# Optimization experiments

Measured on AMD Instinct MI355X. Metric: run time of the kernel, lower is better.

## Reference

```python
import jax, jax.numpy as jnp
import numpy as np

T = 524288
INPUT_LEN = 64
N_MEMORY = 64
OUTPUT_LEN = 32


def setup_inputs() -> dict:
    key = jax.random.key(0)
    k_x, k_w1, k_b1, k_w2, k_b2 = jax.random.split(key, 5)
    s = 0.05  # tf.random_normal_initializer default stddev
    return {
        "inputs": jax.random.normal(k_x, (T, INPUT_LEN), dtype=jnp.float32),
        "W1": s * jax.random.normal(k_w1, (INPUT_LEN, 2 * N_MEMORY), dtype=jnp.float32),
        "B1": s * jax.random.normal(k_b1, (1, 2 * N_MEMORY), dtype=jnp.float32),
        "W2": s * jax.random.normal(k_w2, (N_MEMORY, OUTPUT_LEN), dtype=jnp.float32),
        "B2": s * jax.random.normal(k_b2, (1, OUTPUT_LEN), dtype=jnp.float32),
    }


def reference(inputs, W1, B1, W2, B2):
    n_memory = W2.shape[0]
    # gates: h = sigmoid(x W1 + B1), split into left/right halves  [T, M] each
    h = jax.nn.sigmoid(inputs @ W1 + B1)
    left, right = jnp.split(h, 2, axis=1)
    prod = left * right
    # affine linear recurrence: u_t = prod_{t-1} * u_{t-1} + (1 - left_{t-1}), u_0 = 0
    a = prod[:-1]            # [T-1, M] multiplicative coeffs
    b = 1.0 - left[:-1]      # [T-1, M] additive terms

    def step(u, ab):
        a_t, b_t = ab
        u = a_t * u + b_t
        return u, u

    u0 = jnp.zeros((n_memory,), dtype=inputs.dtype)
    _, us = jax.lax.scan(step, u0, (a, b))
    z = jnp.concatenate([u0[None, :], us], axis=0)  # [T, M]
    out = z @ W2 + B2                               # [T, output_len]
    return out
```

## Files before the change

### kernel.cpp

```cpp
#include <hip/hip_runtime.h>

#define TT    524288
#define CHUNK 512
#define NCH   (TT / CHUNK)
#define SUB   64
#define NSUB  (CHUNK / SUB)

typedef __attribute__((ext_vector_type(8))) short short8;
typedef __attribute__((ext_vector_type(4))) float f32x4;

__device__ __forceinline__ unsigned short f2bf(float f) {
    union { float f; unsigned u; } v; v.f = f;
    unsigned r = v.u + 0x7FFFu + ((v.u >> 16) & 1u);
    return (unsigned short)(r >> 16);
}
__device__ __forceinline__ unsigned packbf2(float a, float b) {
    union { float f; unsigned u; } va, vb; va.f = a; vb.f = b;
    unsigned ra = va.u + 0x7FFFu + ((va.u >> 16) & 1u);
    unsigned rb = vb.u + 0x7FFFu + ((vb.u >> 16) & 1u);
    return (ra >> 16) | (rb & 0xFFFF0000u);
}
__device__ __forceinline__ float2 unpackbf2(unsigned w) {
    union { unsigned u; float f; } a, b;
    a.u = w << 16; b.u = w & 0xFFFF0000u;
    return make_float2(a.f, b.f);
}
__device__ __forceinline__ float sigf(float v) {
    return __builtin_amdgcn_rcpf(1.0f + __expf(-v));
}

union U8 { uint4 u4; short8 s8; };

__global__ __launch_bounds__(256, 3)
void aphase(const float* __restrict__ x, const float* __restrict__ W1,
            const float* __restrict__ B1,
            float* __restrict__ Aout, float* __restrict__ Bout,
            uint4* __restrict__ abg)
{
    __shared__ __align__(16) short W1t[128 * 72];
    __shared__ float    B1s[128];
    __shared__ float    segA[32 * 66], segB[32 * 66];

    const int tid  = threadIdx.x;
    const int c    = blockIdx.x;
    const int wave = tid >> 6;
    const int lane = tid & 63;
    const int quad = lane >> 4;
    const int lr   = lane & 15;

    for (int i = tid; i < 2048; i += 256) {
        float4 w4 = ((const float4*)W1)[i];
        int k = i >> 5, n0 = (i & 31) * 4;
        W1t[(n0 + 0) * 72 + k] = (short)f2bf(w4.x);
        W1t[(n0 + 1) * 72 + k] = (short)f2bf(w4.y);
        W1t[(n0 + 2) * 72 + k] = (short)f2bf(w4.z);
        W1t[(n0 + 3) * 72 + k] = (short)f2bf(w4.w);
    }
    if (tid < 128) B1s[tid] = B1[tid];
    __syncthreads();

    float bb[8];
    #pragma unroll
    for (int j = 0; j < 8; ++j) bb[j] = B1s[j * 16 + lr];

    const float* xbase = x + (size_t)c * CHUNK * 64;

    #define FRAGP(ss, rt) ((const float4*)(xbase + (size_t)(((ss) * 64 + (rt) * 16 + lr)) * 64) + quad * 2)

    const float4* p0 = FRAGP(wave, 0);
    float4 c0 = p0[0], c1 = p0[1], c2 = p0[8], c3 = p0[9];

    const bool h1 = (quad & 1) != 0;
    const bool h2 = (quad & 2) != 0;

    for (int fi = 0; fi < 8; ++fi) {
        const int ss = (fi < 4) ? wave : (wave + 4);
        const int rt = fi & 3;

        U8 ua, ub;
        ua.u4 = make_uint4(packbf2(c0.x, c0.y), packbf2(c0.z, c0.w),
                           packbf2(c1.x, c1.y), packbf2(c1.z, c1.w));
        ub.u4 = make_uint4(packbf2(c2.x, c2.y), packbf2(c2.z, c2.w),
                           packbf2(c3.x, c3.y), packbf2(c3.z, c3.w));
        const short8 a0 = ua.s8, a1 = ub.s8;

        if (fi < 7) {
            const int ns = (fi + 1 < 4) ? wave : (wave + 4);
            const int nr = (fi + 1) & 3;
            const float4* np = FRAGP(ns, nr);
            c0 = np[0]; c1 = np[1]; c2 = np[8]; c3 = np[9];
        }

        f32x4 acc[8];
        #pragma unroll
        for (int j = 0; j < 8; ++j) {
            acc[j][0] = bb[j]; acc[j][1] = bb[j]; acc[j][2] = bb[j]; acc[j][3] = bb[j];
        }
        #pragma unroll
        for (int j = 0; j < 8; ++j) {
            const short8 b0 = *(const short8*)&W1t[(j * 16 + lr) * 72 + quad * 8];
            const short8 b1 = *(const short8*)&W1t[(j * 16 + lr) * 72 + quad * 8 + 32];
            acc[j] = __builtin_amdgcn_mfma_f32_16x16x32_bf16(a0, b0, acc[j], 0, 0, 0);
            acc[j] = __builtin_amdgcn_mfma_f32_16x16x32_bf16(a1, b1, acc[j], 0, 0, 0);
        }

        unsigned pk[4][4];
        #pragma unroll
        for (int j = 0; j < 4; ++j) {
            #pragma unroll
            for (int r = 0; r < 4; ++r) {
                float hl = sigf(acc[j][r]);
                float hr = sigf(acc[j + 4][r]);
                pk[j][r] = packbf2(hl * hr, 1.0f - hl);
            }
        }

        {
            uint4* dstq = abg + ((size_t)((c * NSUB + ss) * 16 + rt * 4 + quad)) * 64 + lr;
            #pragma unroll
            for (int j = 0; j < 4; ++j)
                dstq[j * 16] = make_uint4(pk[j][0], pk[j][1], pk[j][2], pk[j][3]);
        }

        float Aa[4], Ba[4];
        #pragma unroll
        for (int j = 0; j < 4; ++j) {
            float A = 1.0f, Bv = 0.0f;
            #pragma unroll
            for (int r = 0; r < 4; ++r) {
                float2 f = unpackbf2(pk[j][r]);
                Bv = fmaf(f.x, Bv, f.y); A *= f.x;
            }
            Aa[j] = A; Ba[j] = Bv;
        }
        #pragma unroll
        for (int j = 0; j < 4; ++j) {
            float Ap = __shfl_xor(Aa[j], 16);
            float Bp = __shfl_xor(Ba[j], 16);
            float Ahi = h1 ? Aa[j] : Ap;
            float Blo = h1 ? Bp    : Ba[j];
            float Bhi = h1 ? Ba[j] : Bp;
            Aa[j] *= Ap;
            Ba[j] = fmaf(Ahi, Blo, Bhi);

            Ap = __shfl_xor(Aa[j], 32);
            Bp = __shfl_xor(Ba[j], 32);
            Ahi = h2 ? Aa[j] : Ap;
            Blo = h2 ? Bp    : Ba[j];
            Bhi = h2 ? Ba[j] : Bp;
            Aa[j] *= Ap;
            Ba[j] = fmaf(Ahi, Blo, Bhi);
        }
        const float Asel = (quad == 0) ? Aa[0] : (quad == 1) ? Aa[1]
                         : (quad == 2) ? Aa[2] : Aa[3];
        const float Bsel = (quad == 0) ? Ba[0] : (quad == 1) ? Ba[1]
                         : (quad == 2) ? Ba[2] : Ba[3];
        const int band = ss * 4 + rt;
        segA[band * 66 + lane] = Asel;
        segB[band * 66 + lane] = Bsel;
    }
    #undef FRAGP

    __syncthreads();
    if (tid < 64) {
        float sA = 1.0f, sB = 0.0f;
        for (int b = 0; b < 32; ++b) {
            float A2 = segA[b * 66 + tid], B2v = segB[b * 66 + tid];
            sB = fmaf(A2, sB, B2v); sA *= A2;
        }
        Aout[c * 64 + tid] = sA; Bout[c * 64 + tid] = sB;
    }
}

__global__ void carry_scan(const float* __restrict__ Aar, const float* __restrict__ Bar,
                           float* __restrict__ carry)
{
    __shared__ float sA[16 * 66], sB[16 * 66];
    const int tid = threadIdx.x;
    const int ch = tid & 63, seg = tid >> 6;
    const int c0 = seg * (NCH / 16);

    float A = 1.0f, B = 0.0f;
    #pragma unroll 8
    for (int i = 0; i < NCH / 16; ++i) {
        const int idx = c0 + i;
        const float a = Aar[idx * 64 + ch];
        const float b = Bar[idx * 64 + ch];
        B = fmaf(a, B, b); A *= a;
    }
    sA[seg * 66 + ch] = A;
    sB[seg * 66 + ch] = B;
    __syncthreads();

    float u = 0.0f;
    #pragma unroll
    for (int q = 0; q < 15; ++q)
        if (q < seg) u = fmaf(sA[q * 66 + ch], u, sB[q * 66 + ch]);
    #pragma unroll 8
    for (int i = 0; i < NCH / 16; ++i) {
        const int idx = c0 + i;
        carry[idx * 64 + ch] = u;
        u = fmaf(Aar[idx * 64 + ch], u, Bar[idx * 64 + ch]);
    }
}

__global__ __launch_bounds__(256, 4)
void ephase(const uint4* __restrict__ abg, const float* __restrict__ carry,
            const float* __restrict__ W2, const float* __restrict__ B2,
            float* __restrict__ out)
{
    __shared__ __align__(16) short Zs[SUB * 72];
    __shared__ float segA[2 * 4 * 66], segB[2 * 4 * 66];
    __shared__ __align__(16) short W2t[32 * 72];
    __shared__ float B2s[32];
    __shared__ float ucur[2 * 64];

    const int tid  = threadIdx.x;
    const int c    = blockIdx.x;
    const int wave = tid >> 6;
    const int lane = tid & 63;
    const int quad = lane >> 4;
    const int lr   = lane & 15;

    for (int i = tid; i < 512; i += 256) {
        float4 w4 = ((const float4*)W2)[i];
        int k = i >> 3, n0 = (i & 7) * 4;
        W2t[(n0 + 0) * 72 + k] = (short)f2bf(w4.x);
        W2t[(n0 + 1) * 72 + k] = (short)f2bf(w4.y);
        W2t[(n0 + 2) * 72 + k] = (short)f2bf(w4.z);
        W2t[(n0 + 3) * 72 + k] = (short)f2bf(w4.w);
    }
    if (tid < 32) B2s[tid] = B2[tid];
    if (tid < 64) ucur[tid] = carry[c * 64 + tid];

    const uint4* ag = abg + (size_t)c * (NSUB * 16 * 64);
    uint4 r0 = ag[(wave * 4 + 0) * 64 + lane];
    uint4 r1 = ag[(wave * 4 + 1) * 64 + lane];
    uint4 r2 = ag[(wave * 4 + 2) * 64 + lane];
    uint4 r3 = ag[(wave * 4 + 3) * 64 + lane];

    for (int s = 0; s < NSUB; ++s) {
        const int pb = (s & 1) * 264;

        uint4 n0, n1, n2, n3;
        if (s + 1 < NSUB) {
            const uint4* an = ag + (size_t)(s + 1) * (16 * 64);
            n0 = an[(wave * 4 + 0) * 64 + lane];
            n1 = an[(wave * 4 + 1) * 64 + lane];
            n2 = an[(wave * 4 + 2) * 64 + lane];
            n3 = an[(wave * 4 + 3) * 64 + lane];
        }

        float A = 1.0f, Bv = 0.0f; float2 f;
#define CSTEP(W) { f = unpackbf2(W); Bv = fmaf(f.x, Bv, f.y); A *= f.x; }
        CSTEP(r0.x) CSTEP(r0.y) CSTEP(r0.z) CSTEP(r0.w)
        CSTEP(r1.x) CSTEP(r1.y) CSTEP(r1.z) CSTEP(r1.w)
        CSTEP(r2.x) CSTEP(r2.y) CSTEP(r2.z) CSTEP(r2.w)
        CSTEP(r3.x) CSTEP(r3.y) CSTEP(r3.z) CSTEP(r3.w)
#undef CSTEP
        segA[pb + wave * 66 + lane] = A;
        segB[pb + wave * 66 + lane] = Bv;
        __syncthreads();

        float u = ucur[(s & 1) * 64 + lane];
        #pragma unroll
        for (int q = 0; q < 3; ++q)
            if (q < wave) u = fmaf(segA[pb + q * 66 + lane], u, segB[pb + q * 66 + lane]);

        int t = 0;
#define ESTEP(W) { Zs[(wave * 16 + t) * 72 + lane] = (short)f2bf(u); \
                   f = unpackbf2(W); u = fmaf(f.x, u, f.y); ++t; }
        ESTEP(r0.x) ESTEP(r0.y) ESTEP(r0.z) ESTEP(r0.w)
        ESTEP(r1.x) ESTEP(r1.y) ESTEP(r1.z) ESTEP(r1.w)
        ESTEP(r2.x) ESTEP(r2.y) ESTEP(r2.z) ESTEP(r2.w)
        ESTEP(r3.x) ESTEP(r3.y) ESTEP(r3.z) ESTEP(r3.w)
#undef ESTEP
        if (wave == 3) ucur[((s + 1) & 1) * 64 + lane] = u;

        const short8 za0 = *(const short8*)&Zs[(wave * 16 + lr) * 72 + quad * 8];
        const short8 za1 = *(const short8*)&Zs[(wave * 16 + lr) * 72 + quad * 8 + 32];
        const size_t row0g = (size_t)c * CHUNK + (size_t)s * SUB;
        #pragma unroll
        for (int nt = 0; nt < 2; ++nt) {
            f32x4 cc;
            float b = B2s[nt * 16 + lr];
            cc[0] = b; cc[1] = b; cc[2] = b; cc[3] = b;
            const short8 b0 = *(const short8*)&W2t[(nt * 16 + lr) * 72 + quad * 8];
            const short8 b1 = *(const short8*)&W2t[(nt * 16 + lr) * 72 + quad * 8 + 32];
            cc = __builtin_amdgcn_mfma_f32_16x16x32_bf16(za0, b0, cc, 0, 0, 0);
            cc = __builtin_amdgcn_mfma_f32_16x16x32_bf16(za1, b1, cc, 0, 0, 0);
            #pragma unroll
            for (int r = 0; r < 4; ++r) {
                int m = wave * 16 + quad * 4 + r;
                out[(row0g + m) * 32 + nt * 16 + lr] = cc[r];
            }
        }
        if (s + 1 < NSUB) { r0 = n0; r1 = n1; r2 = n2; r3 = n3; }
    }
}

extern "C" void kernel_launch(void* const* d_in, const int* in_sizes, int n_in,
                              void* d_out, int out_size, void* d_ws, size_t ws_size,
                              hipStream_t stream)
{
    const float* x  = (const float*)d_in[0];
    const float* W1 = (const float*)d_in[1];
    const float* B1 = (const float*)d_in[2];
    const float* W2 = (const float*)d_in[3];
    const float* B2 = (const float*)d_in[4];
    float* out = (float*)d_out;

    float* Aar   = (float*)d_ws;
    float* Bar   = Aar + NCH * 64;
    float* carry = Bar + NCH * 64;
    uint4* abg   = (uint4*)(carry + NCH * 64);

    aphase<<<NCH, 256, 0, stream>>>(x, W1, B1, Aar, Bar, abg);
    carry_scan<<<1, 1024, 0, stream>>>(Aar, Bar, carry);
    ephase<<<NCH, 256, 0, stream>>>(abg, carry, W2, B2, out);
}
```

Measured before the change: 296.6 us.

## Stream x tiles via async global-to-LDS DMA with triple buffering and pre-swizzled W1

Moves the W1 transpose and bf16 conversion into a one-block prep kernel that writes an XOR-swizzled layout, which aphase then copies straight into LDS. The x fragment loads become global_load_lds DMA into a per-wave triple buffer, issued two tiles ahead and gated with explicit vmcnt waits, so the loads overlap the MFMA work. Per-band partial scan results are folded in registers per sub-block, shrinking the segment arrays and the final serial combine. In exchange it uses more LDS, lowers the occupancy hint to 2 blocks, and adds an extra kernel launch, and the correctness of the hand-written waitcnt counts is fragile.

```diff
diff --git a/kernel.cpp b/kernel.cpp
--- a/kernel.cpp
+++ b/kernel.cpp
@@ -31,15 +31,37 @@
 
 union U8 { uint4 u4; short8 s8; };
 
-__global__ __launch_bounds__(256, 3)
-void aphase(const float* __restrict__ x, const float* __restrict__ W1,
+__device__ __forceinline__ void gl_lds16(const void* g, void* l) {
+    __builtin_amdgcn_global_load_lds(
+        (__attribute__((address_space(1))) void*)g,
+        (__attribute__((address_space(3))) void*)l, 16, 0, 0);
+}
+
+__global__ void prep(const float* __restrict__ W1, short* __restrict__ w1swz)
+{
+    const int tid = threadIdx.x;
+    for (int i = tid; i < 2048; i += 256) {
+        float4 w4 = ((const float4*)W1)[i];
+        int k = i >> 5, n0 = (i & 31) * 4;
+        int kb = k >> 3, kr = k & 7;
+        float v[4] = { w4.x, w4.y, w4.z, w4.w };
+        #pragma unroll
+        for (int j = 0; j < 4; ++j) {
+            int n = n0 + j;
+            w1swz[n * 64 + ((kb ^ (n & 7)) * 8) + kr] = (short)f2bf(v[j]);
+        }
+    }
+}
+
+__global__ __launch_bounds__(256, 2)
+void aphase(const float* __restrict__ x, const short* __restrict__ w1swz,
             const float* __restrict__ B1,
             float* __restrict__ Aout, float* __restrict__ Bout,
             uint4* __restrict__ abg)
 {
-    __shared__ __align__(16) short W1t[128 * 72];
-    __shared__ float    B1s[128];
-    __shared__ float    segA[32 * 66], segB[32 * 66];
+    __shared__ __align__(16) short W1s[128 * 64];
+    __shared__ __align__(16) float xs[4][3][16 * 64];
+    __shared__ float segA[8 * 65], segB[8 * 65];
 
     const int tid  = threadIdx.x;
     const int c    = blockIdx.x;
@@ -47,35 +69,57 @@
     const int lane = tid & 63;
     const int quad = lane >> 4;
     const int lr   = lane & 15;
-
-    for (int i = tid; i < 2048; i += 256) {
-        float4 w4 = ((const float4*)W1)[i];
-        int k = i >> 5, n0 = (i & 31) * 4;
-        W1t[(n0 + 0) * 72 + k] = (short)f2bf(w4.x);
-        W1t[(n0 + 1) * 72 + k] = (short)f2bf(w4.y);
-        W1t[(n0 + 2) * 72 + k] = (short)f2bf(w4.z);
-        W1t[(n0 + 3) * 72 + k] = (short)f2bf(w4.w);
-    }
-    if (tid < 128) B1s[tid] = B1[tid];
-    __syncthreads();
-
+    const int rlo  = lane >> 4;
+    const int usrc = lane & 15;
+
+    {
+        const uint4* src = (const uint4*)w1swz;
+        uint4* dst = (uint4*)W1s;
+        #pragma unroll
+        for (int i = 0; i < 4; ++i) dst[tid + 256 * i] = src[tid + 256 * i];
+    }
     float bb[8];
     #pragma unroll
-    for (int j = 0; j < 8; ++j) bb[j] = B1s[j * 16 + lr];
+    for (int j = 0; j < 8; ++j) bb[j] = B1[j * 16 + lr];
+    __syncthreads();
 
     const float* xbase = x + (size_t)c * CHUNK * 64;
 
-    #define FRAGP(ss, rt) ((const float4*)(xbase + (size_t)(((ss) * 64 + (rt) * 16 + lr)) * 64) + quad * 2)
-
-    const float4* p0 = FRAGP(wave, 0);
-    float4 c0 = p0[0], c1 = p0[1], c2 = p0[8], c3 = p0[9];
+    #define ISSUE_DMA(TT_, BU_) {                                              \
+        const int ss_ = ((TT_) < 4) ? wave : (wave + 4);                       \
+        const int rt_ = (TT_) & 3;                                             \
+        float* lb_ = &xs[wave][(BU_)][0];                                      \
+        _Pragma("unroll")                                                      \
+        for (int d_ = 0; d_ < 4; ++d_) {                                       \
+            const int rit_ = d_ * 4 + rlo;                                     \
+            const float* g_ = xbase + (size_t)(ss_ * 64 + rt_ * 16 + rit_) * 64\
+                              + ((usrc ^ (rit_ & 7)) << 2);                    \
+            gl_lds16(g_, lb_ + d_ * 256);                                      \
+        } }
+
+    ISSUE_DMA(0, 0)
+    ISSUE_DMA(1, 1)
+    asm volatile("s_waitcnt vmcnt(4)" ::: "memory");
 
     const bool h1 = (quad & 1) != 0;
     const bool h2 = (quad & 2) != 0;
-
+    float sAw = 1.0f, sBw = 0.0f;
+
+    #pragma unroll
     for (int fi = 0; fi < 8; ++fi) {
         const int ss = (fi < 4) ? wave : (wave + 4);
         const int rt = fi & 3;
+        const int bu = fi % 3;
+
+        asm volatile("s_waitcnt vmcnt(8)" ::: "memory");
+        __builtin_amdgcn_sched_barrier(0);
+
+        const float* xr = &xs[wave][bu][0];
+        const int u0 = (quad * 2) ^ (lr & 7);
+        const float4 c0 = *(const float4*)&xr[lr * 64 + u0 * 4];
+        const float4 c1 = *(const float4*)&xr[lr * 64 + (u0 ^ 1) * 4];
+        const float4 c2 = *(const float4*)&xr[lr * 64 + (u0 + 8) * 4];
+        const float4 c3 = *(const float4*)&xr[lr * 64 + ((u0 ^ 1) + 8) * 4];
 
         U8 ua, ub;
         ua.u4 = make_uint4(packbf2(c0.x, c0.y), packbf2(c0.z, c0.w),
@@ -84,22 +128,17 @@
                            packbf2(c3.x, c3.y), packbf2(c3.z, c3.w));
         const short8 a0 = ua.s8, a1 = ub.s8;
 
-        if (fi < 7) {
-            const int ns = (fi + 1 < 4) ? wave : (wave + 4);
-            const int nr = (fi + 1) & 3;
-            const float4* np = FRAGP(ns, nr);
-            c0 = np[0]; c1 = np[1]; c2 = np[8]; c3 = np[9];
-        }
-
         f32x4 acc[8];
         #pragma unroll
         for (int j = 0; j < 8; ++j) {
             acc[j][0] = bb[j]; acc[j][1] = bb[j]; acc[j][2] = bb[j]; acc[j][3] = bb[j];
         }
+        const int ub0 = quad ^ (lr & 7);
         #pragma unroll
         for (int j = 0; j < 8; ++j) {
-            const short8 b0 = *(const short8*)&W1t[(j * 16 + lr) * 72 + quad * 8];
-            const short8 b1 = *(const short8*)&W1t[(j * 16 + lr) * 72 + quad * 8 + 32];
+            const int rw = j * 16 + lr;
+            const short8 b0 = *(const short8*)&W1s[rw * 64 + ub0 * 8];
+            const short8 b1 = *(const short8*)&W1s[rw * 64 + (ub0 ^ 4) * 8];
             acc[j] = __builtin_amdgcn_mfma_f32_16x16x32_bf16(a0, b0, acc[j], 0, 0, 0);
             acc[j] = __builtin_amdgcn_mfma_f32_16x16x32_bf16(a1, b1, acc[j], 0, 0, 0);
         }
@@ -120,6 +159,12 @@
             #pragma unroll
             for (int j = 0; j < 4; ++j)
                 dstq[j * 16] = make_uint4(pk[j][0], pk[j][1], pk[j][2], pk[j][3]);
+        }
+
+        asm volatile("" ::: "memory");
+        {
+            const int t2 = (fi + 2) & 7;
+            ISSUE_DMA(t2, (fi + 2) % 3)
         }
 
         float Aa[4], Ba[4];
@@ -155,17 +200,19 @@
                          : (quad == 2) ? Aa[2] : Aa[3];
         const float Bsel = (quad == 0) ? Ba[0] : (quad == 1) ? Ba[1]
                          : (quad == 2) ? Ba[2] : Ba[3];
-        const int band = ss * 4 + rt;
-        segA[band * 66 + lane] = Asel;
-        segB[band * 66 + lane] = Bsel;
-    }
-    #undef FRAGP
+
+        if (rt == 0) { sAw = Asel; sBw = Bsel; }
+        else         { sBw = fmaf(Asel, sBw, Bsel); sAw *= Asel; }
+        if (rt == 3) { segA[ss * 65 + lane] = sAw; segB[ss * 65 + lane] = sBw; }
+    }
+    #undef ISSUE_DMA
 
     __syncthreads();
     if (tid < 64) {
         float sA = 1.0f, sB = 0.0f;
-        for (int b = 0; b < 32; ++b) {
-            float A2 = segA[b * 66 + tid], B2v = segB[b * 66 + tid];
+        #pragma unroll
+        for (int b = 0; b < 8; ++b) {
+            float A2 = segA[b * 65 + tid], B2v = segB[b * 65 + tid];
             sB = fmaf(A2, sB, B2v); sA *= A2;
         }
         Aout[c * 64 + tid] = sA; Bout[c * 64 + tid] = sB;
@@ -314,8 +361,10 @@
     float* Bar   = Aar + NCH * 64;
     float* carry = Bar + NCH * 64;
     uint4* abg   = (uint4*)(carry + NCH * 64);
-
-    aphase<<<NCH, 256, 0, stream>>>(x, W1, B1, Aar, Bar, abg);
+    short* w1swz = (short*)(abg + (size_t)TT * 16);
+
+    prep<<<1, 256, 0, stream>>>(W1, w1swz);
+    aphase<<<NCH, 256, 0, stream>>>(x, w1swz, B1, Aar, Bar, abg);
     carry_scan<<<1, 1024, 0, stream>>>(Aar, Bar, carry);
     ephase<<<NCH, 256, 0, stream>>>(abg, carry, W2, B2, out);
 }
```

New measurement: 302.9 us. +2.1%, slower.
